# Performance work log

Hardware: AMD Instinct MI355X
Metric: run time of the kernel (lower is better)

The kernel has to match this reference:

```python
import jax, jax.numpy as jnp
import numpy as np

B, S, D, H = 4, 2048, 1024, 16
HD = D // H  # head dim = 64


def setup_inputs() -> dict:
    key = jax.random.key(0)
    ks = jax.random.split(key, 10)
    sd = 1.0 / np.sqrt(D)
    return {
        "x": jax.random.normal(ks[0], (B, S, D), jnp.float32),
        "Wq": jax.random.normal(ks[1], (D, D), jnp.float32) * sd,
        "Wk": jax.random.normal(ks[2], (D, D), jnp.float32) * sd,
        "Wv": jax.random.normal(ks[3], (D, D), jnp.float32) * sd,
        "in_w": jax.random.normal(ks[4], (3 * D, D), jnp.float32) * sd,
        "in_b": jax.random.normal(ks[5], (3 * D,), jnp.float32) * 0.01,
        "out_w": jax.random.normal(ks[6], (D, D), jnp.float32) * sd,
        "out_b": jax.random.normal(ks[7], (D,), jnp.float32) * 0.01,
        "proj_w": jax.random.normal(ks[8], (D, D), jnp.float32) * sd,
        "proj_b": jax.random.normal(ks[9], (D,), jnp.float32) * 0.01,
    }


def _attn_block(x, Wq, Wk, Wv, in_w, in_b, out_w, out_b, proj_w, proj_b):
    b, s, d = x.shape
    # redundant pre-projections (bias-free)
    q = jnp.einsum('bsd,ed->bse', x, Wq)
    k = jnp.einsum('bsd,ed->bse', x, Wk)
    v = jnp.einsum('bsd,ed->bse', x, Wv)
    # MultiheadAttention internal in-projection (with bias)
    wq, wk, wv = in_w[:d], in_w[d:2 * d], in_w[2 * d:]
    bq, bk, bv = in_b[:d], in_b[d:2 * d], in_b[2 * d:]
    Q = jnp.einsum('bse,fe->bsf', q, wq) + bq
    K = jnp.einsum('bse,fe->bsf', k, wk) + bk
    V = jnp.einsum('bse,fe->bsf', v, wv) + bv
    # split heads -> [b, h, s, hd]
    Q = Q.reshape(b, s, H, HD).transpose(0, 2, 1, 3)
    K = K.reshape(b, s, H, HD).transpose(0, 2, 1, 3)
    V = V.reshape(b, s, H, HD).transpose(0, 2, 1, 3)
    scale = 1.0 / np.sqrt(HD)
    scores = jnp.einsum('bhqd,bhkd->bhqk', Q * scale, K)
    # FAITHFUL quirk: float tril mask (ones / zeros) is ADDED to scores,
    # exactly as torch does with a float attn_mask (not a -inf causal mask).
    mask = jnp.tril(jnp.ones((s, s), scores.dtype))
    scores = scores + mask
    A = jax.nn.softmax(scores, axis=-1)
    ctx = jnp.einsum('bhqk,bhkd->bhqd', A, V)
    ctx = ctx.transpose(0, 2, 1, 3).reshape(b, s, d)
    attn = jnp.einsum('bse,fe->bsf', ctx, out_w) + out_b  # out_proj
    out = jnp.einsum('bse,fe->bsf', attn, proj_w) + proj_b  # self.project
    return x + out


def reference(x, Wq, Wk, Wv, in_w, in_b, out_w, out_b, proj_w, proj_b):
    return _attn_block(x, Wq, Wk, Wv, in_w, in_b, out_w, out_b, proj_w, proj_b)
```

## Files before the change

### kernel.cpp

```cpp
#include <hip/hip_runtime.h>
#include <stdint.h>

typedef unsigned short u16;
typedef __attribute__((ext_vector_type(8))) short bfx8;
typedef __attribute__((ext_vector_type(4))) float fx4;
typedef __attribute__((ext_vector_type(2))) unsigned int uint32x2;

static __device__ __forceinline__ u16 f2b(float f) {
  union { float f; uint32_t u; } v; v.f = f;
  uint32_t r = v.u + 0x7fffu + ((v.u >> 16) & 1u);
  return (u16)(r >> 16);
}

static __device__ __forceinline__ uint32_t cvtpk(float lo, float hi) {
  uint32_t r;
  asm("v_cvt_pk_bf16_f32 %0, %1, %2" : "=v"(r) : "v"(lo), "v"(hi));
  return r;
}

static __device__ __forceinline__ float ex2(float x) {
  float r;
  asm("v_exp_f32 %0, %1" : "=v"(r) : "v"(x));
  return r;
}

static __device__ __forceinline__ void gload16(const void* g, void* lds) {
  __builtin_amdgcn_global_load_lds((const __attribute__((address_space(1))) uint32_t*)g,
                                   (__attribute__((address_space(3))) uint32_t*)lds,
                                   16, 0, 0);
}

__global__ __launch_bounds__(256) void f32_to_bf16_k(const float* __restrict__ in,
                                                     u16* __restrict__ out, int n) {
  int i = (blockIdx.x * 256 + threadIdx.x) * 8;
  if (i >= n) return;
  float4 a = *(const float4*)(in + i);
  float4 b = *(const float4*)(in + i + 4);
  bfx8 o;
  o[0]=(short)f2b(a.x); o[1]=(short)f2b(a.y); o[2]=(short)f2b(a.z); o[3]=(short)f2b(a.w);
  o[4]=(short)f2b(b.x); o[5]=(short)f2b(b.y); o[6]=(short)f2b(b.z); o[7]=(short)f2b(b.w);
  *(bfx8*)(out + i) = o;
}

struct TransArgs { const float* in[4]; u16* out[4]; };
__global__ __launch_bounds__(256) void transpose4_k(TransArgs ta) {
  const float* in = ta.in[blockIdx.z];
  u16* out = ta.out[blockIdx.z];
  __shared__ u16 t[64][65];
  const int bx = blockIdx.x * 64, by = blockIdx.y * 64;
  const int tid = threadIdx.x;
#pragma unroll
  for (int i = 0; i < 16; ++i) {
    int idx = tid + i * 256; int r = idx >> 6, c = idx & 63;
    t[c][r] = f2b(in[(size_t)(by + r) * 1024 + bx + c]);
  }
  __syncthreads();
#pragma unroll
  for (int i = 0; i < 16; ++i) {
    int idx = tid + i * 256; int r = idx >> 6, c = idx & 63;
    out[(size_t)(bx + r) * 1024 + by + c] = t[r][c];
  }
}

__global__ __launch_bounds__(256) void make_b2_k(const float* __restrict__ pw,
                                                 const float* __restrict__ ob,
                                                 const float* __restrict__ pb,
                                                 float* __restrict__ b2) {
  const int f = blockIdx.x, tid = threadIdx.x;
  float s = 0.f;
  for (int e = tid; e < 1024; e += 256) s += pw[(size_t)f * 1024 + e] * ob[e];
#pragma unroll
  for (int d = 1; d < 64; d <<= 1) s += __shfl_xor(s, d);
  __shared__ float red[4];
  if ((tid & 63) == 0) red[tid >> 6] = s;
  __syncthreads();
  if (tid == 0) b2[f] = red[0] + red[1] + red[2] + red[3] + pb[f];
}

static __device__ __forceinline__ void gemm_core(const u16* __restrict__ A,
                                                 const u16* __restrict__ Bt,
                                                 int K, int bm, int bn,
                                                 u16* As, u16* Bs, fx4 (&acc)[4][4]) {
  const int tid = threadIdx.x, w = tid >> 6, l = tid & 63, lm = l & 15, lk = l >> 4;
  const int wm = w >> 1, wn = w & 1;
  const int nkt = K >> 6;
  for (int kt = 0; kt < nkt; ++kt) {
#pragma unroll
    for (int i = 0; i < 4; ++i) {
      int off = i * 4096 + w * 1024;
      int loff = off + l * 16;
      int row = loff >> 7, cb = loff & 127;
      gload16((const char*)A + ((size_t)(bm * 128 + row) * K + kt * 64) * 2 + cb,
              (char*)As + off);
      gload16((const char*)Bt + ((size_t)(bn * 128 + row) * K + kt * 64) * 2 + cb,
              (char*)Bs + off);
    }
    __syncthreads();
#pragma unroll
    for (int kk = 0; kk < 2; ++kk) {
      bfx8 a[4], b[4];
#pragma unroll
      for (int mi = 0; mi < 4; ++mi)
        a[mi] = *(const bfx8*)((const char*)As + (wm * 64 + mi * 16 + lm) * 128 + lk * 16 + kk * 64);
#pragma unroll
      for (int nj = 0; nj < 4; ++nj)
        b[nj] = *(const bfx8*)((const char*)Bs + (wn * 64 + nj * 16 + lm) * 128 + lk * 16 + kk * 64);
#pragma unroll
      for (int mi = 0; mi < 4; ++mi)
#pragma unroll
        for (int nj = 0; nj < 4; ++nj)
          acc[mi][nj] = __builtin_amdgcn_mfma_f32_16x16x32_bf16(a[mi], b[nj], acc[mi][nj], 0, 0, 0);
    }
    __syncthreads();
  }
}

struct CombArgs { const u16* A[4]; const u16* Bt[4]; u16* C[4]; };
__global__ __launch_bounds__(256) void gemm_combine_k(CombArgs ca) {
  const int z = blockIdx.z;
  __shared__ u16 As[8192], Bs[8192];
  fx4 acc[4][4];
#pragma unroll
  for (int mi = 0; mi < 4; ++mi)
#pragma unroll
    for (int nj = 0; nj < 4; ++nj) acc[mi][nj] = 0.f;
  gemm_core(ca.A[z], ca.Bt[z], 1024, blockIdx.x, blockIdx.y, As, Bs, acc);
  const int tid = threadIdx.x, w = tid >> 6, l = tid & 63, lm = l & 15, lk = l >> 4;
  const int wm = w >> 1, wn = w & 1;
  u16* C = ca.C[z];
#pragma unroll
  for (int mi = 0; mi < 4; ++mi)
#pragma unroll
    for (int nj = 0; nj < 4; ++nj)
#pragma unroll
      for (int r = 0; r < 4; ++r) {
        int m = blockIdx.x * 128 + wm * 64 + mi * 16 + lk * 4 + r;
        int n = blockIdx.y * 128 + wn * 64 + nj * 16 + lm;
        C[(size_t)m * 1024 + n] = f2b(acc[mi][nj][r]);
      }
}

__global__ __launch_bounds__(256) void gemm_qkv_k(const u16* __restrict__ xb,
                                                  const u16* __restrict__ Wc,
                                                  const float* __restrict__ bias,
                                                  u16* __restrict__ Qh, u16* __restrict__ Kh,
                                                  u16* __restrict__ Vh) {
  __shared__ u16 As[8192], Bs[8192];
  fx4 acc[4][4];
#pragma unroll
  for (int mi = 0; mi < 4; ++mi)
#pragma unroll
    for (int nj = 0; nj < 4; ++nj) acc[mi][nj] = 0.f;
  gemm_core(xb, Wc, 1024, blockIdx.x, blockIdx.y, As, Bs, acc);
  const int tid = threadIdx.x, w = tid >> 6, l = tid & 63, lm = l & 15, lk = l >> 4;
  const int wm = w >> 1, wn = w & 1;
  const int t = (blockIdx.y * 128) >> 10;
  u16* dst = (t == 0) ? Qh : ((t == 1) ? Kh : Vh);
#pragma unroll
  for (int mi = 0; mi < 4; ++mi)
#pragma unroll
    for (int nj = 0; nj < 4; ++nj)
#pragma unroll
      for (int r = 0; r < 4; ++r) {
        int m = blockIdx.x * 128 + wm * 64 + mi * 16 + lk * 4 + r;
        int n = blockIdx.y * 128 + wn * 64 + nj * 16 + lm;
        float v = acc[mi][nj][r] + bias[n];
        int f = n & 1023, h = f >> 6, hd = f & 63, b = m >> 11, s = m & 2047;
        size_t hb = ((size_t)(b * 16 + h)) * 131072;
        size_t idx;
        if (t == 2) {
          int sl = s & 63, st = s >> 6;
          idx = hb + (size_t)st * 4096 +
                (size_t)((sl >> 2) * 256 + (hd >> 4) * 64 + (sl & 3) * 16 + (hd & 15));
        } else if (t == 1) {
          idx = hb + (size_t)s * 64 + (hd ^ ((s & 7) << 3));
        } else {
          idx = hb + (size_t)s * 64 + hd;
        }
        dst[idx] = f2b(v);
      }
}

__global__ __launch_bounds__(256) void gemm_final_k(const u16* __restrict__ ctx,
                                                    const u16* __restrict__ W2,
                                                    const float* __restrict__ b2,
                                                    const float* __restrict__ x,
                                                    float* __restrict__ out) {
  __shared__ u16 As[8192], Bs[8192];
  fx4 acc[4][4];
#pragma unroll
  for (int mi = 0; mi < 4; ++mi)
#pragma unroll
    for (int nj = 0; nj < 4; ++nj) acc[mi][nj] = 0.f;
  gemm_core(ctx, W2, 1024, blockIdx.x, blockIdx.y, As, Bs, acc);
  const int tid = threadIdx.x, w = tid >> 6, l = tid & 63, lm = l & 15, lk = l >> 4;
  const int wm = w >> 1, wn = w & 1;
#pragma unroll
  for (int mi = 0; mi < 4; ++mi)
#pragma unroll
    for (int nj = 0; nj < 4; ++nj)
#pragma unroll
      for (int r = 0; r < 4; ++r) {
        int m = blockIdx.x * 128 + wm * 64 + mi * 16 + lk * 4 + r;
        int n = blockIdx.y * 128 + wn * 64 + nj * 16 + lm;
        size_t idx = (size_t)m * 1024 + n;
        out[idx] = acc[mi][nj][r] + b2[n] + x[idx];
      }
}

#define TRRD(d, IMM) asm volatile("ds_read_b64_tr_b16 %0, %1 offset:" IMM : "=v"(d) : "v"(va))

__global__ __launch_bounds__(256) void attn_k(const u16* __restrict__ Qh,
                                              const u16* __restrict__ Kh,
                                              const u16* __restrict__ Vh,
                                              u16* __restrict__ ctx) {
  const int bh = blockIdx.y, qt = blockIdx.x;
  const int tid = threadIdx.x, w = tid >> 6, l = tid & 63, lm = l & 15, lk = l >> 4;
  __shared__ __align__(16) u16 Ks[2][4096];
  __shared__ __align__(16) u16 Vs[2][4096];
  __shared__ __align__(16) u16 Pl[4][1024];

  const float SC = 0.18033688011112042f;
  const float MA = 1.4426950408889634f;
  const float THR = 11.541560327111708f;

  const size_t base = (size_t)bh * 131072;
  bfx8 qf[2][2];
#pragma unroll
  for (int g = 0; g < 2; ++g) {
    const u16* qp = Qh + base + (size_t)(qt * 128 + g * 64 + w * 16 + lm) * 64;
    qf[g][0] = *(const bfx8*)(qp + lk * 8);
    qf[g][1] = *(const bfx8*)(qp + lk * 8 + 32);
  }
  float m_run[2] = {-INFINITY, -INFINITY};
  float l_part[2] = {0.f, 0.f};
  fx4 accO[2][4];
#pragma unroll
  for (int g = 0; g < 2; ++g)
#pragma unroll
    for (int nj = 0; nj < 4; ++nj) accO[g][nj] = 0.f;

  const char* Kg = (const char*)(Kh + base);
  const char* Vg = (const char*)(Vh + base);
  const int o0 = w * 1024 + l * 16, o1 = o0 + 4096;

  const int swz = (lm & 7) << 4;
  const uint32_t vs_base =
      (uint32_t)(uintptr_t)(__attribute__((address_space(3))) char*)&Vs[0][0];
  const uint32_t vtrb = vs_base + (uint32_t)(lk * 1024 + lm * 8);

  gload16(Kg + o0, (char*)Ks[0] + o0);
  gload16(Kg + o1, (char*)Ks[0] + o1);
  gload16(Vg + o0, (char*)Vs[0] + o0);
  gload16(Vg + o1, (char*)Vs[0] + o1);
  __syncthreads();

  int cur = 0;
  for (int kt = 0; kt < 32; ++kt) {
    if (kt < 31) {
      int nb = cur ^ 1;
      const char* kg = Kg + (kt + 1) * 8192;
      const char* vg = Vg + (kt + 1) * 8192;
      gload16(kg + o0, (char*)Ks[nb] + o0);
      gload16(kg + o1, (char*)Ks[nb] + o1);
      gload16(vg + o0, (char*)Vs[nb] + o0);
      gload16(vg + o1, (char*)Vs[nb] + o1);
    }
    const char* Kc = (const char*)Ks[cur];
    fx4 s[2][4];
#pragma unroll
    for (int g = 0; g < 2; ++g)
#pragma unroll
      for (int nj = 0; nj < 4; ++nj) s[g][nj] = 0.f;
#pragma unroll
    for (int kk = 0; kk < 2; ++kk) {
      bfx8 kf[4];
#pragma unroll
      for (int nj = 0; nj < 4; ++nj)
        kf[nj] = *(const bfx8*)(Kc + nj * 2048 + lm * 128 +
                                (((kk * 4 + lk) ^ (lm & 7)) << 4));
#pragma unroll
      for (int g = 0; g < 2; ++g)
#pragma unroll
        for (int nj = 0; nj < 4; ++nj)
          s[g][nj] = __builtin_amdgcn_mfma_f32_16x16x32_bf16(kf[nj], qf[g][kk], s[g][nj], 0, 0, 0);
    }
#pragma unroll
    for (int g = 0; g < 2; ++g) {
      const int dk = kt - 2 * qt - g;
      if (dk < 0) {
#pragma unroll
        for (int nj = 0; nj < 4; ++nj)
#pragma unroll
          for (int r = 0; r < 4; ++r) s[g][nj][r] = fmaf(s[g][nj][r], SC, MA);
      } else if (dk > 0) {
#pragma unroll
        for (int nj = 0; nj < 4; ++nj)
#pragma unroll
          for (int r = 0; r < 4; ++r) s[g][nj][r] *= SC;
      } else {
        const int qg = qt * 128 + g * 64 + w * 16 + lm;
#pragma unroll
        for (int nj = 0; nj < 4; ++nj)
#pragma unroll
          for (int r = 0; r < 4; ++r) {
            int key = kt * 64 + nj * 16 + lk * 4 + r;
            s[g][nj][r] = s[g][nj][r] * SC + ((key <= qg) ? MA : 0.0f);
          }
      }
      float mx = fmaxf(fmaxf(fmaxf(s[g][0][0], s[g][0][1]), fmaxf(s[g][0][2], s[g][0][3])),
                       fmaxf(fmaxf(s[g][1][0], s[g][1][1]), fmaxf(s[g][1][2], s[g][1][3])));
      mx = fmaxf(mx, fmaxf(fmaxf(fmaxf(s[g][2][0], s[g][2][1]), fmaxf(s[g][2][2], s[g][2][3])),
                           fmaxf(fmaxf(s[g][3][0], s[g][3][1]), fmaxf(s[g][3][2], s[g][3][3]))));
      if (!__all(mx <= m_run[g] + THR)) {
        mx = fmaxf(mx, __shfl_xor(mx, 16));
        mx = fmaxf(mx, __shfl_xor(mx, 32));
        float mn = fmaxf(m_run[g], mx);
        float corr = ex2(m_run[g] - mn);
        m_run[g] = mn;
        l_part[g] *= corr;
#pragma unroll
        for (int r = 0; r < 4; ++r) {
          float cr = __shfl(corr, (l & 48) | (lk * 4 + r));
#pragma unroll
          for (int nj = 0; nj < 4; ++nj) accO[g][nj][r] *= cr;
        }
      }
      float lsum = 0.f;
#pragma unroll
      for (int nj = 0; nj < 4; ++nj)
#pragma unroll
        for (int r = 0; r < 4; ++r) {
          float p = ex2(s[g][nj][r] - m_run[g]);
          s[g][nj][r] = p;
          lsum += p;
        }
      l_part[g] += lsum;
    }
#pragma unroll
    for (int nj = 0; nj < 4; ++nj) {
      uint32x2 pw;
      pw[0] = cvtpk(s[0][nj][0], s[0][nj][1]);
      pw[1] = cvtpk(s[0][nj][2], s[0][nj][3]);
      *(uint32x2*)((char*)Pl[w] + ((lm * 128 + nj * 32 + lk * 8) ^ swz)) = pw;
    }
    uint32x2 tr[2][4][2];
    uint32_t va = vtrb + (uint32_t)(cur * 8192);
    TRRD(tr[0][0][0], "0");    TRRD(tr[0][0][1], "512");
    TRRD(tr[0][1][0], "128");  TRRD(tr[0][1][1], "640");
    TRRD(tr[0][2][0], "256");  TRRD(tr[0][2][1], "768");
    TRRD(tr[0][3][0], "384");  TRRD(tr[0][3][1], "896");
    TRRD(tr[1][0][0], "4096"); TRRD(tr[1][0][1], "4608");
    TRRD(tr[1][1][0], "4224"); TRRD(tr[1][1][1], "4736");
    TRRD(tr[1][2][0], "4352"); TRRD(tr[1][2][1], "4864");
    TRRD(tr[1][3][0], "4480"); TRRD(tr[1][3][1], "4992");
    asm volatile("s_waitcnt lgkmcnt(0)" ::: "memory");
    __builtin_amdgcn_sched_barrier(0);
#pragma unroll
    for (int kk = 0; kk < 2; ++kk) {
      bfx8 pf = *(const bfx8*)((char*)Pl[w] + ((lm * 128 + kk * 64 + lk * 16) ^ swz));
#pragma unroll
      for (int nj = 0; nj < 4; ++nj) {
        union { uint32x2 u2[2]; bfx8 v; } u;
        u.u2[0] = tr[kk][nj][0];
        u.u2[1] = tr[kk][nj][1];
        accO[0][nj] = __builtin_amdgcn_mfma_f32_16x16x32_bf16(pf, u.v, accO[0][nj], 0, 0, 0);
      }
    }
#pragma unroll
    for (int nj = 0; nj < 4; ++nj) {
      uint32x2 pw;
      pw[0] = cvtpk(s[1][nj][0], s[1][nj][1]);
      pw[1] = cvtpk(s[1][nj][2], s[1][nj][3]);
      *(uint32x2*)((char*)Pl[w] + ((lm * 128 + nj * 32 + lk * 8) ^ swz)) = pw;
    }
#pragma unroll
    for (int kk = 0; kk < 2; ++kk) {
      bfx8 pf = *(const bfx8*)((char*)Pl[w] + ((lm * 128 + kk * 64 + lk * 16) ^ swz));
#pragma unroll
      for (int nj = 0; nj < 4; ++nj) {
        union { uint32x2 u2[2]; bfx8 v; } u;
        u.u2[0] = tr[kk][nj][0];
        u.u2[1] = tr[kk][nj][1];
        accO[1][nj] = __builtin_amdgcn_mfma_f32_16x16x32_bf16(pf, u.v, accO[1][nj], 0, 0, 0);
      }
    }
    __syncthreads();
    cur ^= 1;
  }

  const int b = bh >> 4, h = bh & 15;
#pragma unroll
  for (int g = 0; g < 2; ++g) {
    float lt = l_part[g];
    lt += __shfl_xor(lt, 16);
    lt += __shfl_xor(lt, 32);
#pragma unroll
    for (int r = 0; r < 4; ++r) {
      float li = __shfl(lt, (l & 48) | (lk * 4 + r));
      float inv = 1.0f / li;
      int q = qt * 128 + g * 64 + w * 16 + lk * 4 + r;
#pragma unroll
      for (int nj = 0; nj < 4; ++nj)
        ctx[((size_t)b * 2048 + q) * 1024 + h * 64 + nj * 16 + lm] = f2b(accO[g][nj][r] * inv);
    }
  }
}

extern "C" void kernel_launch(void* const* d_in, const int* in_sizes, int n_in,
                              void* d_out, int out_size, void* d_ws, size_t ws_size,
                              hipStream_t stream) {
  (void)in_sizes; (void)n_in; (void)out_size; (void)ws_size;
  const float* x      = (const float*)d_in[0];
  const float* Wq     = (const float*)d_in[1];
  const float* Wk     = (const float*)d_in[2];
  const float* Wv     = (const float*)d_in[3];
  const float* in_w   = (const float*)d_in[4];
  const float* in_b   = (const float*)d_in[5];
  const float* out_w  = (const float*)d_in[6];
  const float* out_b  = (const float*)d_in[7];
  const float* proj_w = (const float*)d_in[8];
  const float* proj_b = (const float*)d_in[9];
  float* out = (float*)d_out;

  char* ws = (char*)d_ws;
  const size_t MB = 1ull << 20;
  u16* xb   = (u16*)(ws);
  u16* ctx  = xb;
  u16* Qh   = (u16*)(ws + 16 * MB);
  u16* Kh   = (u16*)(ws + 32 * MB);
  u16* Vh   = (u16*)(ws + 48 * MB);
  u16* inwb = Kh;
  u16* tmpT = Vh;
  u16* pwb  = (u16*)(ws + 48 * MB + 8 * MB);
  u16* Wc   = (u16*)(ws + 64 * MB);
  u16* W2   = (u16*)(ws + 70 * MB);
  float* b2 = (float*)(ws + 72 * MB);

  f32_to_bf16_k<<<4096, 256, 0, stream>>>(x, xb, 8388608);
  f32_to_bf16_k<<<1536, 256, 0, stream>>>(in_w, inwb, 3145728);
  f32_to_bf16_k<<<512, 256, 0, stream>>>(proj_w, pwb, 1048576);

  TransArgs ta;
  ta.in[0] = Wq; ta.in[1] = Wk; ta.in[2] = Wv; ta.in[3] = out_w;
  for (int z = 0; z < 4; ++z) ta.out[z] = tmpT + (size_t)z * 1048576;
  transpose4_k<<<dim3(16, 16, 4), 256, 0, stream>>>(ta);

  CombArgs ca;
  ca.A[0] = inwb; ca.A[1] = inwb + 1048576; ca.A[2] = inwb + 2097152; ca.A[3] = pwb;
  for (int z = 0; z < 4; ++z) ca.Bt[z] = tmpT + (size_t)z * 1048576;
  ca.C[0] = Wc; ca.C[1] = Wc + 1048576; ca.C[2] = Wc + 2097152; ca.C[3] = W2;
  gemm_combine_k<<<dim3(8, 8, 4), 256, 0, stream>>>(ca);

  make_b2_k<<<1024, 256, 0, stream>>>(proj_w, out_b, proj_b, b2);

  gemm_qkv_k<<<dim3(64, 24), 256, 0, stream>>>(xb, Wc, in_b, Qh, Kh, Vh);
  attn_k<<<dim3(16, 64), 256, 0, stream>>>(Qh, Kh, Vh, ctx);
  gemm_final_k<<<dim3(64, 8), 256, 0, stream>>>(ctx, W2, b2, x, out);
}
```

Before: 299.3 us.

## Triple-buffer attention K/V loads with vmcnt waits, setprio, and XCD-aware block remap

Moves the attention kernel's K/V staging from double to triple buffering. Loads are issued two tiles ahead and waited on with explicit vmcnt counts plus raw s_barrier, replacing the full __syncthreads at the end of each iteration. MFMA sections are wrapped in s_setprio to favour matrix work, and the 2D grid becomes a 1D grid with a remap that spreads consecutive blocks across the 8 XCDs so that blocks of the same head share an L2. The cost is more LDS per block, which may reduce occupancy, and vmcnt accounting that depends on each thread issuing exactly four loads per stage.

```diff
diff --git a/kernel.cpp b/kernel.cpp
--- a/kernel.cpp
+++ b/kernel.cpp
@@ -214,10 +214,12 @@
                                               const u16* __restrict__ Kh,
                                               const u16* __restrict__ Vh,
                                               u16* __restrict__ ctx) {
-  const int bh = blockIdx.y, qt = blockIdx.x;
+  const int bl = blockIdx.x;
+  const int wk = (bl & 7) * 128 + (bl >> 3);
+  const int bh = wk >> 4, qt = wk & 15;
   const int tid = threadIdx.x, w = tid >> 6, l = tid & 63, lm = l & 15, lk = l >> 4;
-  __shared__ __align__(16) u16 Ks[2][4096];
-  __shared__ __align__(16) u16 Vs[2][4096];
+  __shared__ __align__(16) u16 Ks[3][4096];
+  __shared__ __align__(16) u16 Vs[3][4096];
   __shared__ __align__(16) u16 Pl[4][1024];
 
   const float SC = 0.18033688011112042f;
@@ -249,29 +251,34 @@
       (uint32_t)(uintptr_t)(__attribute__((address_space(3))) char*)&Vs[0][0];
   const uint32_t vtrb = vs_base + (uint32_t)(lk * 1024 + lm * 8);
 
-  gload16(Kg + o0, (char*)Ks[0] + o0);
-  gload16(Kg + o1, (char*)Ks[0] + o1);
-  gload16(Vg + o0, (char*)Vs[0] + o0);
-  gload16(Vg + o1, (char*)Vs[0] + o1);
-  __syncthreads();
-
-  int cur = 0;
+#define STAGE(t, s)                                        \
+  {                                                        \
+    const char* kg_ = Kg + (t) * 8192;                     \
+    const char* vg_ = Vg + (t) * 8192;                     \
+    gload16(kg_ + o0, (char*)Ks[s] + o0);                  \
+    gload16(kg_ + o1, (char*)Ks[s] + o1);                  \
+    gload16(vg_ + o0, (char*)Vs[s] + o0);                  \
+    gload16(vg_ + o1, (char*)Vs[s] + o1);                  \
+  }
+
+  STAGE(0, 0);
+  STAGE(1, 1);
+  asm volatile("s_waitcnt vmcnt(4)" ::: "memory");
+  __builtin_amdgcn_s_barrier();
+  __builtin_amdgcn_sched_barrier(0);
+
+  int s0 = 0, s1 = 1, s2 = 2;
   for (int kt = 0; kt < 32; ++kt) {
-    if (kt < 31) {
-      int nb = cur ^ 1;
-      const char* kg = Kg + (kt + 1) * 8192;
-      const char* vg = Vg + (kt + 1) * 8192;
-      gload16(kg + o0, (char*)Ks[nb] + o0);
-      gload16(kg + o1, (char*)Ks[nb] + o1);
-      gload16(vg + o0, (char*)Vs[nb] + o0);
-      gload16(vg + o1, (char*)Vs[nb] + o1);
-    }
-    const char* Kc = (const char*)Ks[cur];
+    if (kt + 2 < 32) STAGE(kt + 2, s2);
+    __builtin_amdgcn_sched_barrier(0);
+
+    const char* Kc = (const char*)Ks[s0];
     fx4 s[2][4];
 #pragma unroll
     for (int g = 0; g < 2; ++g)
 #pragma unroll
       for (int nj = 0; nj < 4; ++nj) s[g][nj] = 0.f;
+    __builtin_amdgcn_s_setprio(1);
 #pragma unroll
     for (int kk = 0; kk < 2; ++kk) {
       bfx8 kf[4];
@@ -285,6 +292,7 @@
         for (int nj = 0; nj < 4; ++nj)
           s[g][nj] = __builtin_amdgcn_mfma_f32_16x16x32_bf16(kf[nj], qf[g][kk], s[g][nj], 0, 0, 0);
     }
+    __builtin_amdgcn_s_setprio(0);
 #pragma unroll
     for (int g = 0; g < 2; ++g) {
       const int dk = kt - 2 * qt - g;
@@ -345,7 +353,7 @@
       *(uint32x2*)((char*)Pl[w] + ((lm * 128 + nj * 32 + lk * 8) ^ swz)) = pw;
     }
     uint32x2 tr[2][4][2];
-    uint32_t va = vtrb + (uint32_t)(cur * 8192);
+    uint32_t va = vtrb + (uint32_t)(s0 * 8192);
     TRRD(tr[0][0][0], "0");    TRRD(tr[0][0][1], "512");
     TRRD(tr[0][1][0], "128");  TRRD(tr[0][1][1], "640");
     TRRD(tr[0][2][0], "256");  TRRD(tr[0][2][1], "768");
@@ -356,6 +364,7 @@
     TRRD(tr[1][3][0], "4480"); TRRD(tr[1][3][1], "4992");
     asm volatile("s_waitcnt lgkmcnt(0)" ::: "memory");
     __builtin_amdgcn_sched_barrier(0);
+    __builtin_amdgcn_s_setprio(1);
 #pragma unroll
     for (int kk = 0; kk < 2; ++kk) {
       bfx8 pf = *(const bfx8*)((char*)Pl[w] + ((lm * 128 + kk * 64 + lk * 16) ^ swz));
@@ -367,6 +376,7 @@
         accO[0][nj] = __builtin_amdgcn_mfma_f32_16x16x32_bf16(pf, u.v, accO[0][nj], 0, 0, 0);
       }
     }
+    __builtin_amdgcn_s_setprio(0);
 #pragma unroll
     for (int nj = 0; nj < 4; ++nj) {
       uint32x2 pw;
@@ -374,6 +384,7 @@
       pw[1] = cvtpk(s[1][nj][2], s[1][nj][3]);
       *(uint32x2*)((char*)Pl[w] + ((lm * 128 + nj * 32 + lk * 8) ^ swz)) = pw;
     }
+    __builtin_amdgcn_s_setprio(1);
 #pragma unroll
     for (int kk = 0; kk < 2; ++kk) {
       bfx8 pf = *(const bfx8*)((char*)Pl[w] + ((lm * 128 + kk * 64 + lk * 16) ^ swz));
@@ -385,9 +396,17 @@
         accO[1][nj] = __builtin_amdgcn_mfma_f32_16x16x32_bf16(pf, u.v, accO[1][nj], 0, 0, 0);
       }
     }
-    __syncthreads();
-    cur ^= 1;
-  }
+    __builtin_amdgcn_s_setprio(0);
+
+    if (kt < 31) {
+      if (kt < 30) asm volatile("s_waitcnt vmcnt(4)" ::: "memory");
+      else         asm volatile("s_waitcnt vmcnt(0)" ::: "memory");
+      __builtin_amdgcn_s_barrier();
+      __builtin_amdgcn_sched_barrier(0);
+    }
+    int tswp = s0; s0 = s1; s1 = s2; s2 = tswp;
+  }
+#undef STAGE
 
   const int b = bh >> 4, h = bh & 15;
 #pragma unroll
@@ -455,6 +474,6 @@
   make_b2_k<<<1024, 256, 0, stream>>>(proj_w, out_b, proj_b, b2);
 
   gemm_qkv_k<<<dim3(64, 24), 256, 0, stream>>>(xb, Wc, in_b, Qh, Kh, Vh);
-  attn_k<<<dim3(16, 64), 256, 0, stream>>>(Qh, Kh, Vh, ctx);
+  attn_k<<<1024, 256, 0, stream>>>(Qh, Kh, Vh, ctx);
   gemm_final_k<<<dim3(64, 8), 256, 0, stream>>>(ctx, W2, b2, x, out);
 }
```

Measured after the change: 294.3 us. No clear change (-1.7%).
